# Optimization experiments

Hardware: AMD Instinct MI355X
Metric: run time of the kernel (lower is better)

Reference implementation:

```python
import jax, jax.numpy as jnp
import numpy as np

B, L, D, H = 2, 2048, 2048, 16
C = D // H  # head dim = 128
EPS = 1e-5


def setup_inputs() -> dict:
    key = jax.random.key(0)
    k1, k2, k3, k4 = jax.random.split(key, 4)
    scale = 1.0 / np.sqrt(D)
    return {
        "x": jax.random.normal(k1, (B, L, D), dtype=jnp.float32),
        "theta": jax.random.uniform(k2, (B, L, D // 2), dtype=jnp.float32) * 6.2831853,
        "w_qkv": jax.random.normal(k3, (3 * D, D), dtype=jnp.float32) * scale,
        "w_y": jax.random.normal(k4, (D, D), dtype=jnp.float32) * scale,
        "b_y": jnp.zeros((D,), dtype=jnp.float32),
    }


def _rms_norm(t):
    # RMSNorm over last dim, eps=1e-5, no affine
    return t * jax.lax.rsqrt(jnp.mean(t * t, axis=-1, keepdims=True) + EPS)


def _apply_rope(q, k, theta):
    # q, k: (B, H, L, C); theta: (B, H, L, C//2)
    qr, qi = q[..., 0::2], q[..., 1::2]
    kr, ki = k[..., 0::2], k[..., 1::2]
    cos_t, sin_t = jnp.cos(theta), jnp.sin(theta)
    q_rot = jnp.stack((qr * cos_t - qi * sin_t, qr * sin_t + qi * cos_t), axis=-1).reshape(q.shape)
    k_rot = jnp.stack((kr * cos_t - ki * sin_t, kr * sin_t + ki * cos_t), axis=-1).reshape(k.shape)
    return q_rot, k_rot


def reference(x, theta, w_qkv, w_y, b_y):
    # QKV projection: (B, L, 3D)
    qkv = jnp.einsum("bld,ed->ble", x, w_qkv)
    # rearrange '... L (n H C) -> n ... H L C'
    qkv = qkv.reshape(B, L, 3, H, C).transpose(2, 0, 3, 1, 4)  # (3, B, H, L, C)
    q, k, v = qkv[0], qkv[1], qkv[2]
    q, k = _rms_norm(q), _rms_norm(k)
    # theta: (B, L, H*C/2) -> (B, H, L, C/2)
    th = theta.reshape(B, L, H, C // 2).transpose(0, 2, 1, 3)
    q, k = _apply_rope(q, k, th)
    # scaled dot-product attention
    scores = jnp.einsum("bhqc,bhkc->bhqk", q, k) / np.sqrt(C).astype(np.float32)
    attn = jax.nn.softmax(scores, axis=-1)
    y = jnp.einsum("bhqk,bhkc->bhqc", attn, v)
    # (B, H, L, C) -> (B, L, H*C)
    y = y.transpose(0, 2, 1, 3).reshape(B, L, D)
    return jnp.einsum("bld,ed->ble", y, w_y) + b_y
```

## Files before the change

### kernel.cpp

```cpp
#include <hip/hip_runtime.h>
#include <stdint.h>

typedef uint16_t u16;
typedef __attribute__((ext_vector_type(8))) short bf16x8;
typedef __attribute__((ext_vector_type(4))) float f32x4;


__device__ __forceinline__ u16 f2bf(float f) {
  uint32_t u = __builtin_bit_cast(uint32_t, f);
  u += 0x7fffu + ((u >> 16) & 1u);
  return (u16)(u >> 16);
}
__device__ __forceinline__ float bf2f(u16 h) {
  return __builtin_bit_cast(float, (uint32_t)h << 16);
}
__device__ __forceinline__ uint32_t pack2bf(float a, float b) {
  uint32_t ua = __builtin_bit_cast(uint32_t, a) + 0x7fffu;
  uint32_t ub = __builtin_bit_cast(uint32_t, b) + 0x7fffu;
  return (ua >> 16) | (ub & 0xffff0000u);
}
__device__ __forceinline__ void gl_lds16(const u16* g, u16* l) {
  __builtin_amdgcn_global_load_lds((const __attribute__((address_space(1))) uint32_t*)g,
                                   (__attribute__((address_space(3))) uint32_t*)l, 16, 0, 0);
}

__global__ __launch_bounds__(256) void castk(const float* __restrict__ in,
                                             u16* __restrict__ out, int n) {
  int idx = (blockIdx.x * 256 + threadIdx.x) * 4;
  int stride = gridDim.x * 256 * 4;
  for (int i = idx; i < n; i += stride) {
    float4 v = *(const float4*)(in + i);
    uint32_t lo = (uint32_t)f2bf(v.x) | ((uint32_t)f2bf(v.y) << 16);
    uint32_t hi = (uint32_t)f2bf(v.z) | ((uint32_t)f2bf(v.w) << 16);
    *(uint2*)(out + i) = make_uint2(lo, hi);
  }
}

__global__ __launch_bounds__(512, 1) void gemm8_qkv(
    const u16* __restrict__ A, const u16* __restrict__ Bw,
    u16* __restrict__ qb, u16* __restrict__ kb, u16* __restrict__ vt) {
  __shared__ u16 sm[57344];
  const int K = 2048;
  const int tid = threadIdx.x, lane = tid & 63;
  const int wid = tid >> 6, g = lane >> 4, lr = lane & 15;
  const int wm = wid >> 2, wn = wid & 3;
  const int m0 = blockIdx.y * 256, n0 = blockIdx.x * 192;
  const int srow = tid >> 3, sjs = (tid & 7) ^ (srow & 7);

  auto stA = [&](int buf, int kt, int R) {
    gl_lds16(A + (size_t)(m0 + R + srow) * K + kt * 64 + sjs * 8,
             &sm[buf * 28672 + R * 64 + tid * 8]);
  };
  auto stB = [&](int buf, int kt, int R) {
    gl_lds16(Bw + (size_t)(n0 + R + srow) * K + kt * 64 + sjs * 8,
             &sm[buf * 28672 + 16384 + R * 64 + tid * 8]);
  };
  auto rdA = [&](const u16* As, int mf, int ks) {
    int ra = wm * 128 + mf * 16 + lr;
    return *(const bf16x8*)&As[ra * 64 + (((ks * 4 + g) ^ (ra & 7)) * 8)];
  };
  auto rdB = [&](const u16* Bs, int nf, int ks) {
    int rb = wn * 48 + nf * 16 + lr;
    return *(const bf16x8*)&Bs[rb * 64 + (((ks * 4 + g) ^ (rb & 7)) * 8)];
  };

  f32x4 acc[8][3] = {};
  bf16x8 bc[3][2], fP0[4][2], fP1[4][2];

  stB(0, 0, 0); stB(0, 0, 64); stB(0, 0, 128);
  stA(0, 0, 0); stA(0, 0, 128);
  stA(0, 0, 64); stA(0, 0, 192);
  asm volatile("s_waitcnt vmcnt(2)" ::: "memory");
  __builtin_amdgcn_s_barrier();
  {
    const u16* As0 = &sm[0];
#pragma unroll
    for (int i = 0; i < 4; ++i)
#pragma unroll
      for (int ks = 0; ks < 2; ++ks) fP0[i][ks] = rdA(As0, i, ks);
  }

  for (int t = 0; t < 32; ++t) {
    const int cur = t & 1, nxt = cur ^ 1;
    const int kn = (t < 31) ? t + 1 : 31;
    const u16* Asc = &sm[cur * 28672];
    const u16* Bsc = &sm[cur * 28672 + 16384];
    const u16* Asn = &sm[nxt * 28672];

    stB(nxt, kn, 0); stB(nxt, kn, 64); stB(nxt, kn, 128);
    stA(nxt, kn, 0); stA(nxt, kn, 128);
    asm volatile("s_waitcnt vmcnt(5)" ::: "memory");
    __builtin_amdgcn_s_barrier();
#pragma unroll
    for (int nf = 0; nf < 3; ++nf)
#pragma unroll
      for (int ks = 0; ks < 2; ++ks) bc[nf][ks] = rdB(Bsc, nf, ks);
#pragma unroll
    for (int i = 0; i < 4; ++i)
#pragma unroll
      for (int ks = 0; ks < 2; ++ks) fP1[i][ks] = rdA(Asc, 4 + i, ks);
    __builtin_amdgcn_s_setprio(1);
#pragma unroll
    for (int i = 0; i < 4; ++i)
#pragma unroll
      for (int nf = 0; nf < 3; ++nf) {
        acc[i][nf] = __builtin_amdgcn_mfma_f32_16x16x32_bf16(
            fP0[i][0], bc[nf][0], acc[i][nf], 0, 0, 0);
        acc[i][nf] = __builtin_amdgcn_mfma_f32_16x16x32_bf16(
            fP0[i][1], bc[nf][1], acc[i][nf], 0, 0, 0);
      }
    __builtin_amdgcn_s_setprio(0);

    stA(nxt, kn, 64); stA(nxt, kn, 192);
    asm volatile("s_waitcnt vmcnt(2)" ::: "memory");
    __builtin_amdgcn_s_barrier();
#pragma unroll
    for (int i = 0; i < 4; ++i)
#pragma unroll
      for (int ks = 0; ks < 2; ++ks) fP0[i][ks] = rdA(Asn, i, ks);
    __builtin_amdgcn_s_setprio(1);
#pragma unroll
    for (int i = 0; i < 4; ++i)
#pragma unroll
      for (int nf = 0; nf < 3; ++nf) {
        acc[4 + i][nf] = __builtin_amdgcn_mfma_f32_16x16x32_bf16(
            fP1[i][0], bc[nf][0], acc[4 + i][nf], 0, 0, 0);
        acc[4 + i][nf] = __builtin_amdgcn_mfma_f32_16x16x32_bf16(
            fP1[i][1], bc[nf][1], acc[4 + i][nf], 0, 0, 0);
      }
    __builtin_amdgcn_s_setprio(0);
  }
  asm volatile("s_waitcnt vmcnt(0)" ::: "memory");

#pragma unroll
  for (int mf = 0; mf < 8; ++mf)
#pragma unroll
    for (int nf = 0; nf < 3; ++nf) {
      int n = n0 + wn * 48 + nf * 16 + lr;
      int s = n >> 11, h = (n >> 7) & 15, cb = n & 127;
#pragma unroll
      for (int r = 0; r < 4; ++r) {
        int m = m0 + wm * 128 + mf * 16 + g * 4 + r;
        int b = m >> 11, lp = m & 2047;
        u16 val = f2bf(acc[mf][nf][r]);
        if (s == 0)
          qb[(size_t)((b * 16 + h) * 2048 + lp) * 128 + cb] = val;
        else if (s == 1)
          kb[(size_t)((b * 16 + h) * 2048 + lp) * 128 + cb] = val;
        else
          vt[(size_t)((b * 16 + h) * 128 + cb) * 2048 + lp] = val;
      }
    }
}

__global__ __launch_bounds__(512, 1) void gemm_out(
    const u16* __restrict__ A, const u16* __restrict__ Bw,
    float* __restrict__ out, const float* __restrict__ bias) {
  __shared__ u16 sm[49152];
  const int K = 2048;
  const int tid = threadIdx.x, lane = tid & 63;
  const int wid = tid >> 6, g = lane >> 4, lr = lane & 15;
  const int wm = wid >> 2, wn = wid & 3;
  const int m0 = blockIdx.y * 256, n0 = blockIdx.x * 128;
  const int srow = tid >> 3, sjs = (tid & 7) ^ (srow & 7);

  auto stA = [&](int buf, int kt, int R) {
    gl_lds16(A + (size_t)(m0 + R + srow) * K + kt * 64 + sjs * 8,
             &sm[buf * 24576 + R * 64 + tid * 8]);
  };
  auto stB = [&](int buf, int kt, int R) {
    gl_lds16(Bw + (size_t)(n0 + R + srow) * K + kt * 64 + sjs * 8,
             &sm[buf * 24576 + 16384 + R * 64 + tid * 8]);
  };
  auto rdA = [&](const u16* As, int mf, int ks) {
    int ra = wm * 128 + mf * 16 + lr;
    return *(const bf16x8*)&As[ra * 64 + (((ks * 4 + g) ^ (ra & 7)) * 8)];
  };
  auto rdB = [&](const u16* Bs, int nf, int ks) {
    int rb = wn * 32 + nf * 16 + lr;
    return *(const bf16x8*)&Bs[rb * 64 + (((ks * 4 + g) ^ (rb & 7)) * 8)];
  };

  f32x4 acc[8][2] = {};
  bf16x8 bc[2][2], fP0[4][2], fP1[4][2];

  stB(0, 0, 0); stB(0, 0, 64);
  stA(0, 0, 0); stA(0, 0, 128);
  stA(0, 0, 64); stA(0, 0, 192);
  asm volatile("s_waitcnt vmcnt(2)" ::: "memory");
  __builtin_amdgcn_s_barrier();
  {
    const u16* As0 = &sm[0];
#pragma unroll
    for (int i = 0; i < 4; ++i)
#pragma unroll
      for (int ks = 0; ks < 2; ++ks) fP0[i][ks] = rdA(As0, i, ks);
  }

  for (int t = 0; t < 32; ++t) {
    const int cur = t & 1, nxt = cur ^ 1;
    const int kn = (t < 31) ? t + 1 : 31;
    const u16* Asc = &sm[cur * 24576];
    const u16* Bsc = &sm[cur * 24576 + 16384];
    const u16* Asn = &sm[nxt * 24576];

    stB(nxt, kn, 0); stB(nxt, kn, 64);
    stA(nxt, kn, 0); stA(nxt, kn, 128);
    asm volatile("s_waitcnt vmcnt(4)" ::: "memory");
    __builtin_amdgcn_s_barrier();
#pragma unroll
    for (int nf = 0; nf < 2; ++nf)
#pragma unroll
      for (int ks = 0; ks < 2; ++ks) bc[nf][ks] = rdB(Bsc, nf, ks);
#pragma unroll
    for (int i = 0; i < 4; ++i)
#pragma unroll
      for (int ks = 0; ks < 2; ++ks) fP1[i][ks] = rdA(Asc, 4 + i, ks);
    __builtin_amdgcn_s_setprio(1);
#pragma unroll
    for (int i = 0; i < 4; ++i)
#pragma unroll
      for (int nf = 0; nf < 2; ++nf) {
        acc[i][nf] = __builtin_amdgcn_mfma_f32_16x16x32_bf16(
            fP0[i][0], bc[nf][0], acc[i][nf], 0, 0, 0);
        acc[i][nf] = __builtin_amdgcn_mfma_f32_16x16x32_bf16(
            fP0[i][1], bc[nf][1], acc[i][nf], 0, 0, 0);
      }
    __builtin_amdgcn_s_setprio(0);

    stA(nxt, kn, 64); stA(nxt, kn, 192);
    asm volatile("s_waitcnt vmcnt(2)" ::: "memory");
    __builtin_amdgcn_s_barrier();
#pragma unroll
    for (int i = 0; i < 4; ++i)
#pragma unroll
      for (int ks = 0; ks < 2; ++ks) fP0[i][ks] = rdA(Asn, i, ks);
    __builtin_amdgcn_s_setprio(1);
#pragma unroll
    for (int i = 0; i < 4; ++i)
#pragma unroll
      for (int nf = 0; nf < 2; ++nf) {
        acc[4 + i][nf] = __builtin_amdgcn_mfma_f32_16x16x32_bf16(
            fP1[i][0], bc[nf][0], acc[4 + i][nf], 0, 0, 0);
        acc[4 + i][nf] = __builtin_amdgcn_mfma_f32_16x16x32_bf16(
            fP1[i][1], bc[nf][1], acc[4 + i][nf], 0, 0, 0);
      }
    __builtin_amdgcn_s_setprio(0);
  }
  asm volatile("s_waitcnt vmcnt(0)" ::: "memory");

#pragma unroll
  for (int mf = 0; mf < 8; ++mf)
#pragma unroll
    for (int nf = 0; nf < 2; ++nf) {
      int n = n0 + wn * 32 + nf * 16 + lr;
      float bv = bias[n];
#pragma unroll
      for (int r = 0; r < 4; ++r) {
        int m = m0 + wm * 128 + mf * 16 + g * 4 + r;
        out[(size_t)m * 2048 + n] = acc[mf][nf][r] + bv;
      }
    }
}

__global__ __launch_bounds__(256) void qk_fix(u16* __restrict__ qb, u16* __restrict__ kb,
                                              const float* __restrict__ theta) {
  const int row = blockIdx.x * 4 + (threadIdx.x >> 6);
  const int lane = threadIdx.x & 63;
  const int bh = row >> 11, l = row & 2047;
  const int b = bh >> 4, h = bh & 15;
  float th = theta[(size_t)(b * 2048 + l) * 1024 + h * 64 + lane];
  float sn, cs;
  __sincosf(th, &sn, &cs);
#pragma unroll
  for (int which = 0; which < 2; ++which) {
    u16* buf = which ? kb : qb;
    uint32_t* p = (uint32_t*)(buf + (size_t)row * 128) + lane;
    uint32_t v = *p;
    float x0 = bf2f((u16)(v & 0xffff)), x1 = bf2f((u16)(v >> 16));
    float ss = x0 * x0 + x1 * x1;
#pragma unroll
    for (int m = 1; m <= 32; m <<= 1) ss += __shfl_xor(ss, m);
    float rn = rsqrtf(ss * (1.0f / 128.0f) + 1e-5f);
    if (which == 0) rn *= 0.12751743f;
    x0 *= rn;
    x1 *= rn;
    float y0 = x0 * cs - x1 * sn;
    float y1 = x0 * sn + x1 * cs;
    *p = (uint32_t)f2bf(y0) | ((uint32_t)f2bf(y1) << 16);
  }
}

__global__ __launch_bounds__(512, 1) void attn_k(const u16* __restrict__ qb,
                                                 const u16* __restrict__ kb,
                                                 const u16* __restrict__ vt,
                                                 u16* __restrict__ yb) {
  __shared__ u16 sm[49152];
  const int gid = blockIdx.x;
  const int bh = (gid & 7) * 4 + ((gid >> 3) & 3);
  const int qtile = gid >> 5;
  const int b = bh >> 4, h = bh & 15;
  const int tid = threadIdx.x, lane = tid & 63, wid = tid >> 6;
  const int g = lane >> 4, lr = lane & 15;
  const int q0 = qtile * 256 + wid * 32;

  bf16x8 qf[2][4];
#pragma unroll
  for (int qs = 0; qs < 2; ++qs) {
    const u16* qrow = qb + (size_t)(bh * 2048 + q0 + qs * 16 + lr) * 128;
#pragma unroll
    for (int ks = 0; ks < 4; ++ks) qf[qs][ks] = *(const bf16x8*)&qrow[ks * 32 + g * 8];
  }

  auto stage = [&](int buf, int kv) {
#pragma unroll
    for (int i = 0; i < 2; ++i) {
      int ci = i * 512 + tid;
      int row = ci >> 4, j = ci & 15;
      gl_lds16(kb + (size_t)(bh * 2048 + kv + row) * 128 + (j ^ (row & 7)) * 8,
               &sm[buf * 8192 + ci * 8]);
    }
#pragma unroll
    for (int i = 0; i < 2; ++i) {
      int ci = i * 512 + tid;
      int row = ci >> 3, j = ci & 7;
      gl_lds16(vt + (size_t)(bh * 128 + row) * 2048 + kv + (j ^ (row & 7)) * 8,
               &sm[24576 + buf * 8192 + ci * 8]);
    }
  };

  f32x4 acc[2][8] = {};
  float mrun[2] = {-1e30f, -1e30f}, lrun[2] = {0.f, 0.f};
  const int sA = (2 * (g & 1)) * 16 + lr, sB = sA + 16;
  const bool hi2 = (g >> 1) != 0;

  stage(0, 0);
  stage(1, 64);
  asm volatile("s_waitcnt vmcnt(4)" ::: "memory");
  __builtin_amdgcn_s_barrier();

  int cur = 0;
  for (int t = 0; t < 32; ++t) {
    if (t < 31) {
      int nb = (cur == 0) ? 2 : cur - 1;
      int kvn = ((t < 30) ? t + 2 : 31) * 64;
      stage(nb, kvn);
    }
    const u16* Ks = &sm[cur * 8192];
    const u16* Vs = &sm[24576 + cur * 8192];

    f32x4 st[2][4] = {};
#pragma unroll
    for (int ks = 0; ks < 4; ++ks) {
      bf16x8 kf[4];
#pragma unroll
      for (int kt = 0; kt < 4; ++kt) {
        int row = kt * 16 + lr;
        kf[kt] = *(const bf16x8*)&Ks[row * 128 + (((ks * 4 + g) ^ (row & 7)) * 8)];
      }
#pragma unroll
      for (int kt = 0; kt < 4; ++kt)
#pragma unroll
        for (int qs = 0; qs < 2; ++qs)
          st[qs][kt] =
              __builtin_amdgcn_mfma_f32_16x16x32_bf16(kf[kt], qf[qs][ks], st[qs][kt], 0, 0, 0);
    }

    float pmax[2];
#pragma unroll
    for (int qs = 0; qs < 2; ++qs) {
      float m01 = fmaxf(fmaxf(st[qs][0][0], st[qs][0][1]), fmaxf(st[qs][0][2], st[qs][0][3]));
      float m23 = fmaxf(fmaxf(st[qs][1][0], st[qs][1][1]), fmaxf(st[qs][1][2], st[qs][1][3]));
      float m45 = fmaxf(fmaxf(st[qs][2][0], st[qs][2][1]), fmaxf(st[qs][2][2], st[qs][2][3]));
      float m67 = fmaxf(fmaxf(st[qs][3][0], st[qs][3][1]), fmaxf(st[qs][3][2], st[qs][3][3]));
      float mx = fmaxf(fmaxf(m01, m23), fmaxf(m45, m67));
      mx = fmaxf(mx, __shfl_xor(mx, 16));
      mx = fmaxf(mx, __shfl_xor(mx, 32));
      pmax[qs] = mx;
    }
    float need = fmaxf(pmax[0] - mrun[0], pmax[1] - mrun[1]);
    if (!__all(need <= 8.0f)) {
#pragma unroll
      for (int qs = 0; qs < 2; ++qs) {
        float mnew = fmaxf(mrun[qs], pmax[qs]);
        float corr = __builtin_amdgcn_exp2f(mrun[qs] - mnew);
        lrun[qs] *= corr;
        mrun[qs] = mnew;
#pragma unroll
        for (int ct = 0; ct < 8; ++ct) {
          acc[qs][ct][0] *= corr;
          acc[qs][ct][1] *= corr;
          acc[qs][ct][2] *= corr;
          acc[qs][ct][3] *= corr;
        }
      }
    }
    uint32_t pw[2][4][2];
#pragma unroll
    for (int qs = 0; qs < 2; ++qs) {
      float rsum = 0.f;
#pragma unroll
      for (int kt = 0; kt < 4; ++kt)
#pragma unroll
        for (int hf = 0; hf < 2; ++hf) {
          float e0 = __builtin_amdgcn_exp2f(st[qs][kt][2 * hf] - mrun[qs]);
          float e1 = __builtin_amdgcn_exp2f(st[qs][kt][2 * hf + 1] - mrun[qs]);
          rsum += e0 + e1;
          pw[qs][kt][hf] = pack2bf(e0, e1);
        }
      rsum += __shfl_xor(rsum, 16);
      rsum += __shfl_xor(rsum, 32);
      lrun[qs] += rsum;
    }

#pragma unroll
    for (int ks2 = 0; ks2 < 2; ++ks2) {
      bf16x8 pf[2];
#pragma unroll
      for (int qs = 0; qs < 2; ++qs) {
        uint32_t a0 = __shfl(pw[qs][ks2 * 2][0], sA);
        uint32_t a1 = __shfl(pw[qs][ks2 * 2][1], sA);
        uint32_t a2 = __shfl(pw[qs][ks2 * 2][0], sB);
        uint32_t a3 = __shfl(pw[qs][ks2 * 2][1], sB);
        uint32_t b0 = __shfl(pw[qs][ks2 * 2 + 1][0], sA);
        uint32_t b1 = __shfl(pw[qs][ks2 * 2 + 1][1], sA);
        uint32_t b2 = __shfl(pw[qs][ks2 * 2 + 1][0], sB);
        uint32_t b3 = __shfl(pw[qs][ks2 * 2 + 1][1], sB);
        union {
          uint32_t u[4];
          bf16x8 v;
        } tt;
        tt.u[0] = hi2 ? b0 : a0;
        tt.u[1] = hi2 ? b1 : a1;
        tt.u[2] = hi2 ? b2 : a2;
        tt.u[3] = hi2 ? b3 : a3;
        pf[qs] = tt.v;
      }
#pragma unroll
      for (int ct = 0; ct < 8; ++ct) {
        int row = ct * 16 + lr;
        bf16x8 vf = *(const bf16x8*)&Vs[row * 64 + (((ks2 * 4 + g) ^ (row & 7)) * 8)];
#pragma unroll
        for (int qs = 0; qs < 2; ++qs)
          acc[qs][ct] = __builtin_amdgcn_mfma_f32_16x16x32_bf16(vf, pf[qs], acc[qs][ct], 0, 0, 0);
      }
    }
    if (t < 31) {
      asm volatile("s_waitcnt vmcnt(4)" ::: "memory");
      __builtin_amdgcn_s_barrier();
    }
    cur = (cur == 2) ? 0 : cur + 1;
  }
  asm volatile("s_waitcnt vmcnt(0)" ::: "memory");

#pragma unroll
  for (int qs = 0; qs < 2; ++qs) {
    float inv = 1.f / lrun[qs];
    const size_t orow = (size_t)(b * 2048 + q0 + qs * 16 + lr) * 2048 + h * 128;
#pragma unroll
    for (int ct = 0; ct < 8; ++ct) {
      uint32_t lo = pack2bf(acc[qs][ct][0] * inv, acc[qs][ct][1] * inv);
      uint32_t hi = pack2bf(acc[qs][ct][2] * inv, acc[qs][ct][3] * inv);
      *(uint2*)&yb[orow + ct * 16 + g * 4] = make_uint2(lo, hi);
    }
  }
}

extern "C" void kernel_launch(void* const* d_in, const int* in_sizes, int n_in,
                              void* d_out, int out_size, void* d_ws, size_t ws_size,
                              hipStream_t stream) {
  const float* x = (const float*)d_in[0];
  const float* theta = (const float*)d_in[1];
  const float* wqkv = (const float*)d_in[2];
  const float* wy = (const float*)d_in[3];
  const float* by = (const float*)d_in[4];
  float* out = (float*)d_out;
  char* ws = (char*)d_ws;
  u16* xb  = (u16*)(ws + 0);
  u16* wqb = (u16*)(ws + 16777216);
  u16* wyb = (u16*)(ws + 41943040);
  u16* qb  = (u16*)(ws + 50331648);
  u16* kb  = (u16*)(ws + 67108864);
  u16* vt  = (u16*)(ws + 83886080);
  u16* yb  = (u16*)(ws + 100663296);

  castk<<<2048, 256, 0, stream>>>(x, xb, 2 * 2048 * 2048);
  castk<<<2048, 256, 0, stream>>>(wqkv, wqb, 3 * 2048 * 2048);
  castk<<<1024, 256, 0, stream>>>(wy, wyb, 2048 * 2048);

  gemm8_qkv<<<dim3(32, 16), 512, 0, stream>>>(xb, wqb, qb, kb, vt);
  qk_fix<<<16384, 256, 0, stream>>>(qb, kb, theta);
  attn_k<<<256, 512, 0, stream>>>(qb, kb, vt, yb);
  gemm_out<<<dim3(16, 16), 512, 0, stream>>>(yb, wyb, out, by);
}
```

Measured before the change: 285.1 us.

## Software-pipeline QK^T of next tile with softmax and PV of current tile

```diff
diff --git a/kernel.cpp b/kernel.cpp
--- a/kernel.cpp
+++ b/kernel.cpp
@@ -328,6 +328,24 @@
                &sm[24576 + buf * 8192 + ci * 8]);
     }
   };
+  auto qk = [&](int buf, f32x4 st[2][4]) {
+    const u16* Ks = &sm[buf * 8192];
+#pragma unroll
+    for (int ks = 0; ks < 4; ++ks) {
+      bf16x8 kf[4];
+#pragma unroll
+      for (int kt = 0; kt < 4; ++kt) {
+        int row = kt * 16 + lr;
+        kf[kt] = *(const bf16x8*)&Ks[row * 128 + (((ks * 4 + g) ^ (row & 7)) * 8)];
+      }
+#pragma unroll
+      for (int kt = 0; kt < 4; ++kt)
+#pragma unroll
+        for (int qs = 0; qs < 2; ++qs)
+          st[qs][kt] =
+              __builtin_amdgcn_mfma_f32_16x16x32_bf16(kf[kt], qf[qs][ks], st[qs][kt], 0, 0, 0);
+    }
+  };
 
   f32x4 acc[2][8] = {};
   float mrun[2] = {-1e30f, -1e30f}, lrun[2] = {0.f, 0.f};
@@ -339,118 +357,101 @@
   asm volatile("s_waitcnt vmcnt(4)" ::: "memory");
   __builtin_amdgcn_s_barrier();
 
-  int cur = 0;
-  for (int t = 0; t < 32; ++t) {
-    if (t < 31) {
-      int nb = (cur == 0) ? 2 : cur - 1;
-      int kvn = ((t < 30) ? t + 2 : 31) * 64;
-      stage(nb, kvn);
-    }
-    const u16* Ks = &sm[cur * 8192];
-    const u16* Vs = &sm[24576 + cur * 8192];
-
-    f32x4 st[2][4] = {};
-#pragma unroll
-    for (int ks = 0; ks < 4; ++ks) {
-      bf16x8 kf[4];
-#pragma unroll
-      for (int kt = 0; kt < 4; ++kt) {
-        int row = kt * 16 + lr;
-        kf[kt] = *(const bf16x8*)&Ks[row * 128 + (((ks * 4 + g) ^ (row & 7)) * 8)];
-      }
-#pragma unroll
-      for (int kt = 0; kt < 4; ++kt)
-#pragma unroll
-        for (int qs = 0; qs < 2; ++qs)
-          st[qs][kt] =
-              __builtin_amdgcn_mfma_f32_16x16x32_bf16(kf[kt], qf[qs][ks], st[qs][kt], 0, 0, 0);
-    }
-
-    float pmax[2];
-#pragma unroll
-    for (int qs = 0; qs < 2; ++qs) {
-      float m01 = fmaxf(fmaxf(st[qs][0][0], st[qs][0][1]), fmaxf(st[qs][0][2], st[qs][0][3]));
-      float m23 = fmaxf(fmaxf(st[qs][1][0], st[qs][1][1]), fmaxf(st[qs][1][2], st[qs][1][3]));
-      float m45 = fmaxf(fmaxf(st[qs][2][0], st[qs][2][1]), fmaxf(st[qs][2][2], st[qs][2][3]));
-      float m67 = fmaxf(fmaxf(st[qs][3][0], st[qs][3][1]), fmaxf(st[qs][3][2], st[qs][3][3]));
-      float mx = fmaxf(fmaxf(m01, m23), fmaxf(m45, m67));
-      mx = fmaxf(mx, __shfl_xor(mx, 16));
-      mx = fmaxf(mx, __shfl_xor(mx, 32));
-      pmax[qs] = mx;
-    }
-    float need = fmaxf(pmax[0] - mrun[0], pmax[1] - mrun[1]);
-    if (!__all(need <= 8.0f)) {
-#pragma unroll
-      for (int qs = 0; qs < 2; ++qs) {
-        float mnew = fmaxf(mrun[qs], pmax[qs]);
-        float corr = __builtin_amdgcn_exp2f(mrun[qs] - mnew);
-        lrun[qs] *= corr;
-        mrun[qs] = mnew;
-#pragma unroll
-        for (int ct = 0; ct < 8; ++ct) {
-          acc[qs][ct][0] *= corr;
-          acc[qs][ct][1] *= corr;
-          acc[qs][ct][2] *= corr;
-          acc[qs][ct][3] *= corr;
-        }
-      }
-    }
-    uint32_t pw[2][4][2];
-#pragma unroll
-    for (int qs = 0; qs < 2; ++qs) {
-      float rsum = 0.f;
-#pragma unroll
-      for (int kt = 0; kt < 4; ++kt)
-#pragma unroll
-        for (int hf = 0; hf < 2; ++hf) {
-          float e0 = __builtin_amdgcn_exp2f(st[qs][kt][2 * hf] - mrun[qs]);
-          float e1 = __builtin_amdgcn_exp2f(st[qs][kt][2 * hf + 1] - mrun[qs]);
-          rsum += e0 + e1;
-          pw[qs][kt][hf] = pack2bf(e0, e1);
-        }
-      rsum += __shfl_xor(rsum, 16);
-      rsum += __shfl_xor(rsum, 32);
-      lrun[qs] += rsum;
-    }
-
-#pragma unroll
-    for (int ks2 = 0; ks2 < 2; ++ks2) {
-      bf16x8 pf[2];
-#pragma unroll
-      for (int qs = 0; qs < 2; ++qs) {
-        uint32_t a0 = __shfl(pw[qs][ks2 * 2][0], sA);
-        uint32_t a1 = __shfl(pw[qs][ks2 * 2][1], sA);
-        uint32_t a2 = __shfl(pw[qs][ks2 * 2][0], sB);
-        uint32_t a3 = __shfl(pw[qs][ks2 * 2][1], sB);
-        uint32_t b0 = __shfl(pw[qs][ks2 * 2 + 1][0], sA);
-        uint32_t b1 = __shfl(pw[qs][ks2 * 2 + 1][1], sA);
-        uint32_t b2 = __shfl(pw[qs][ks2 * 2 + 1][0], sB);
-        uint32_t b3 = __shfl(pw[qs][ks2 * 2 + 1][1], sB);
-        union {
-          uint32_t u[4];
-          bf16x8 v;
-        } tt;
-        tt.u[0] = hi2 ? b0 : a0;
-        tt.u[1] = hi2 ? b1 : a1;
-        tt.u[2] = hi2 ? b2 : a2;
-        tt.u[3] = hi2 ? b3 : a3;
-        pf[qs] = tt.v;
-      }
-#pragma unroll
-      for (int ct = 0; ct < 8; ++ct) {
-        int row = ct * 16 + lr;
-        bf16x8 vf = *(const bf16x8*)&Vs[row * 64 + (((ks2 * 4 + g) ^ (row & 7)) * 8)];
-#pragma unroll
-        for (int qs = 0; qs < 2; ++qs)
-          acc[qs][ct] = __builtin_amdgcn_mfma_f32_16x16x32_bf16(vf, pf[qs], acc[qs][ct], 0, 0, 0);
-      }
-    }
-    if (t < 31) {
-      asm volatile("s_waitcnt vmcnt(4)" ::: "memory");
-      __builtin_amdgcn_s_barrier();
-    }
-    cur = (cur == 2) ? 0 : cur + 1;
-  }
+  f32x4 stE[2][4] = {}, stO[2][4] = {};
+  qk(0, stE);
+
+#define ATILE(T, CUR3, NXT3, OVW3, ST_CUR, ST_NXT)                                   \
+  {                                                                                  \
+    if ((T) < 31) stage(OVW3, (((T) < 30) ? (T) + 2 : 31) * 64);                     \
+    asm volatile("s_waitcnt vmcnt(4)" ::: "memory");                                 \
+    __builtin_amdgcn_s_barrier();                                                    \
+    if ((T) < 31) {                                                                  \
+      _Pragma("unroll") for (int qs = 0; qs < 2; ++qs)                               \
+          _Pragma("unroll") for (int kt = 0; kt < 4; ++kt) ST_NXT[qs][kt] = (f32x4){};\
+      qk(NXT3, ST_NXT);                                                              \
+    }                                                                                \
+    float pmax[2];                                                                   \
+    _Pragma("unroll") for (int qs = 0; qs < 2; ++qs) {                               \
+      float m01 = fmaxf(fmaxf(ST_CUR[qs][0][0], ST_CUR[qs][0][1]),                   \
+                        fmaxf(ST_CUR[qs][0][2], ST_CUR[qs][0][3]));                  \
+      float m23 = fmaxf(fmaxf(ST_CUR[qs][1][0], ST_CUR[qs][1][1]),                   \
+                        fmaxf(ST_CUR[qs][1][2], ST_CUR[qs][1][3]));                  \
+      float m45 = fmaxf(fmaxf(ST_CUR[qs][2][0], ST_CUR[qs][2][1]),                   \
+                        fmaxf(ST_CUR[qs][2][2], ST_CUR[qs][2][3]));                  \
+      float m67 = fmaxf(fmaxf(ST_CUR[qs][3][0], ST_CUR[qs][3][1]),                   \
+                        fmaxf(ST_CUR[qs][3][2], ST_CUR[qs][3][3]));                  \
+      float mx = fmaxf(fmaxf(m01, m23), fmaxf(m45, m67));                            \
+      mx = fmaxf(mx, __shfl_xor(mx, 16));                                            \
+      mx = fmaxf(mx, __shfl_xor(mx, 32));                                            \
+      pmax[qs] = mx;                                                                 \
+    }                                                                                \
+    float need = fmaxf(pmax[0] - mrun[0], pmax[1] - mrun[1]);                        \
+    if (!__all(need <= 8.0f)) {                                                      \
+      _Pragma("unroll") for (int qs = 0; qs < 2; ++qs) {                             \
+        float mnew = fmaxf(mrun[qs], pmax[qs]);                                      \
+        float corr = __builtin_amdgcn_exp2f(mrun[qs] - mnew);                        \
+        lrun[qs] *= corr;                                                            \
+        mrun[qs] = mnew;                                                             \
+        _Pragma("unroll") for (int ct = 0; ct < 8; ++ct) {                           \
+          acc[qs][ct][0] *= corr; acc[qs][ct][1] *= corr;                            \
+          acc[qs][ct][2] *= corr; acc[qs][ct][3] *= corr;                            \
+        }                                                                            \
+      }                                                                              \
+    }                                                                                \
+    uint32_t pw[2][4][2];                                                            \
+    _Pragma("unroll") for (int qs = 0; qs < 2; ++qs) {                               \
+      float rsum = 0.f;                                                              \
+      _Pragma("unroll") for (int kt = 0; kt < 4; ++kt)                               \
+          _Pragma("unroll") for (int hf = 0; hf < 2; ++hf) {                         \
+        float e0 = __builtin_amdgcn_exp2f(ST_CUR[qs][kt][2 * hf] - mrun[qs]);        \
+        float e1 = __builtin_amdgcn_exp2f(ST_CUR[qs][kt][2 * hf + 1] - mrun[qs]);    \
+        rsum += e0 + e1;                                                             \
+        pw[qs][kt][hf] = pack2bf(e0, e1);                                            \
+      }                                                                              \
+      rsum += __shfl_xor(rsum, 16);                                                  \
+      rsum += __shfl_xor(rsum, 32);                                                  \
+      lrun[qs] += rsum;                                                              \
+    }                                                                                \
+    const u16* Vs = &sm[24576 + (CUR3)*8192];                                        \
+    _Pragma("unroll") for (int ks2 = 0; ks2 < 2; ++ks2) {                            \
+      bf16x8 pf[2];                                                                  \
+      _Pragma("unroll") for (int qs = 0; qs < 2; ++qs) {                             \
+        uint32_t a0 = __shfl(pw[qs][ks2 * 2][0], sA);                                \
+        uint32_t a1 = __shfl(pw[qs][ks2 * 2][1], sA);                                \
+        uint32_t a2 = __shfl(pw[qs][ks2 * 2][0], sB);                                \
+        uint32_t a3 = __shfl(pw[qs][ks2 * 2][1], sB);                                \
+        uint32_t b0 = __shfl(pw[qs][ks2 * 2 + 1][0], sA);                            \
+        uint32_t b1 = __shfl(pw[qs][ks2 * 2 + 1][1], sA);                            \
+        uint32_t b2 = __shfl(pw[qs][ks2 * 2 + 1][0], sB);                            \
+        uint32_t b3 = __shfl(pw[qs][ks2 * 2 + 1][1], sB);                            \
+        union { uint32_t u[4]; bf16x8 v; } tt;                                       \
+        tt.u[0] = hi2 ? b0 : a0; tt.u[1] = hi2 ? b1 : a1;                            \
+        tt.u[2] = hi2 ? b2 : a2; tt.u[3] = hi2 ? b3 : a3;                            \
+        pf[qs] = tt.v;                                                               \
+      }                                                                              \
+      _Pragma("unroll") for (int ct = 0; ct < 8; ++ct) {                             \
+        int row = ct * 16 + lr;                                                      \
+        bf16x8 vf = *(const bf16x8*)&Vs[row * 64 + (((ks2 * 4 + g) ^ (row & 7)) * 8)];\
+        _Pragma("unroll") for (int qs = 0; qs < 2; ++qs)                             \
+          acc[qs][ct] =                                                              \
+              __builtin_amdgcn_mfma_f32_16x16x32_bf16(vf, pf[qs], acc[qs][ct], 0, 0, 0);\
+      }                                                                              \
+    }                                                                                \
+    __builtin_amdgcn_s_barrier();                                                    \
+  }
+
+  for (int tt = 0; tt < 5; ++tt) {
+    const int t0 = tt * 6;
+    ATILE(t0 + 0, 0, 1, 2, stE, stO);
+    ATILE(t0 + 1, 1, 2, 0, stO, stE);
+    ATILE(t0 + 2, 2, 0, 1, stE, stO);
+    ATILE(t0 + 3, 0, 1, 2, stO, stE);
+    ATILE(t0 + 4, 1, 2, 0, stE, stO);
+    ATILE(t0 + 5, 2, 0, 1, stO, stE);
+  }
+  ATILE(30, 0, 1, 2, stE, stO);
+  ATILE(31, 1, 2, 0, stO, stE);
+#undef ATILE
   asm volatile("s_waitcnt vmcnt(0)" ::: "memory");
 
 #pragma unroll
```

Result: slower. 300.4 us (+5.4%).
